# Performance work log

Hardware: AMD Instinct MI355X
Metric: run time of the kernel (lower is better)

The kernel has to match this reference:

```python
import jax, jax.numpy as jnp
import numpy as np

BSZ, NW, T = 16, 1024, 3072   # batch, max words per seq, padded byte length
BED, WED = 128, 512           # byte_embed_dim, word_embed_dim
NH = 2                        # highway layers per block
VOCAB = 256 + 4 + 4
BPE_MASK_IDX = 4


def _conv1d(x, W, b):
    # x: [B, T, Cin], W: [k, Cin, Cout]
    y = jax.lax.conv_general_dilated(x, W, window_strides=(1,), padding='SAME',
                                     dimension_numbers=('NWC', 'WIO', 'NWC'))
    return y + b


def _highway(x, Ws, bs):
    # Ws: [NH, 2D, D], bs: [NH, 2D]; AllenNLP-style highway
    for i in range(NH):
        proj = x @ Ws[i].T + bs[i]
        h, g = jnp.split(proj, 2, axis=-1)
        g = jax.nn.sigmoid(g)
        x = g * jax.nn.relu(h) + (1.0 - g) * x
    return x


def setup_inputs() -> dict:
    rng = np.random.default_rng(0)
    pool_lengths = rng.integers(1, 4, size=(BSZ, NW)).astype(np.int64)  # all >=1 -> npools == NW
    src_lengths = pool_lengths.sum(axis=1)
    byte_tokens = np.zeros((BSZ, T), dtype=np.int64)
    for b in range(BSZ):
        L = int(src_lengths[b])
        byte_tokens[b, :L] = rng.integers(4, 260, size=L)
    pos = np.arange(T)[None, :]
    bpe_mask = (rng.random((BSZ, T)) < 0.3) & (pos < src_lengths[:, None])

    key = jax.random.key(0)
    ks = jax.random.split(key, 12)
    s = 0.02
    tok_emb = jax.random.normal(ks[0], (VOCAB, BED), jnp.float32) * s
    tok_emb = tok_emb.at[0].set(0.0)  # padding_idx = 0
    return {
        'byte_tokens': jnp.asarray(byte_tokens),
        'bpe_mask': jnp.asarray(bpe_mask),
        'pool_lengths': jnp.asarray(pool_lengths),
        'tok_emb': tok_emb,
        'conv0_W': jax.random.normal(ks[1], (3, BED, WED), jnp.float32) * s,
        'conv0_b': jnp.zeros((WED,), jnp.float32),
        'conv1_W': jax.random.normal(ks[2], (3, WED, WED), jnp.float32) * s,
        'conv1_b': jnp.zeros((WED,), jnp.float32),
        'hw0_W': jax.random.normal(ks[3], (NH, 2 * WED, WED), jnp.float32) * s,
        'hw0_b': jnp.zeros((NH, 2 * WED), jnp.float32),
        'hw1_W': jax.random.normal(ks[4], (NH, 2 * WED, WED), jnp.float32) * s,
        'hw1_b': jnp.zeros((NH, 2 * WED), jnp.float32),
        'proj_W': jax.random.normal(ks[5], (WED, WED), jnp.float32) * s,
        'proj_b': jnp.zeros((WED,), jnp.float32),
    }


def reference(byte_tokens, bpe_mask, pool_lengths, tok_emb,
              conv0_W, conv0_b, conv1_W, conv1_b,
              hw0_W, hw0_b, hw1_W, hw1_b, proj_W, proj_b):
    # byte embedding + bpe-marker embedding (index 0 row is zero => no-op where mask is False)
    x = tok_emb[byte_tokens] + tok_emb[jnp.where(bpe_mask, BPE_MASK_IDX, 0)]
    # ConvHighway block 0 (no residual)
    x = _highway(jax.nn.relu(_conv1d(x, conv0_W, conv0_b)), hw0_W, hw0_b)
    # ConvHighway block 1 (residual_conv=True); dropout is identity in eval
    x = _highway(jax.nn.relu(_conv1d(x, conv1_W, conv1_b)) + x, hw1_W, hw1_b)

    # ragged per-word max pool via segment_max (replaces the python double loop)
    cum = jnp.cumsum(pool_lengths, axis=1)                 # [B, NW]
    pos = jnp.arange(T)
    seg = jax.vmap(lambda c: jnp.searchsorted(c, pos, side='right'))(cum)  # [B, T]
    src_len = cum[:, -1]
    valid = pos[None, :] < src_len[:, None]
    gid = jnp.where(valid, jnp.arange(BSZ)[:, None] * NW + jnp.clip(seg, 0, NW - 1), BSZ * NW)
    pooled = jax.ops.segment_max(x.reshape(BSZ * T, WED), gid.reshape(-1),
                                 num_segments=BSZ * NW + 1)
    pooled = pooled[:BSZ * NW].reshape(BSZ, NW, WED)
    pooled = jnp.where(jnp.isfinite(pooled), pooled, 0.0)  # empty pools -> 0 like new_zeros
    return pooled @ proj_W.T + proj_b
```

## Files before the change

### kernel.cpp

```cpp
#include <hip/hip_runtime.h>
#include <hip/hip_bf16.h>
#include <math.h>

typedef __attribute__((ext_vector_type(8))) short short8v;
typedef __attribute__((ext_vector_type(4))) float float4v;

namespace {
constexpr int kBSZ = 16;
constexpr int kNW  = 1024;
constexpr int kT   = 3072;
constexpr int kBED = 128;
constexpr int kWED = 512;
constexpr int kR   = kBSZ * kT;
constexpr int kMP  = kBSZ * kNW;
}

__device__ __forceinline__ unsigned short f2b(float x) {
  unsigned int u = __float_as_uint(x);
  u = u + 0x7FFFu + ((u >> 16) & 1u);
  return (unsigned short)(u >> 16);
}
__device__ __forceinline__ float b2f(unsigned short u) {
  return __uint_as_float(((unsigned int)u) << 16);
}

__device__ __forceinline__ void async16(void* l, const void* g) {
  __builtin_amdgcn_global_load_lds(
      (const __attribute__((address_space(1))) void*)g,
      (__attribute__((address_space(3))) void*)l, 16, 0, 0);
}

__global__ __launch_bounds__(256) void k_embed(
    const int* __restrict__ tok, const int* __restrict__ msk,
    const float* __restrict__ emb, unsigned short* __restrict__ out) {
  int idx = blockIdx.x * 256 + threadIdx.x;
  int row = idx >> 5, c4 = idx & 31;
  const float4* e4 = (const float4*)emb;
  float4 a = e4[tok[row] * 32 + c4];
  float4 b = e4[(msk[row] ? 4 : 0) * 32 + c4];
  ushort4 o;
  o.x = f2b(a.x + b.x); o.y = f2b(a.y + b.y);
  o.z = f2b(a.z + b.z); o.w = f2b(a.w + b.w);
  ((ushort4*)out)[idx] = o;
}

__global__ __launch_bounds__(256) void k_wt_conv(
    const float* __restrict__ W, unsigned short* __restrict__ o, int CIN) {
  int idx = blockIdx.x * 256 + threadIdx.x;
  if (idx >= 3 * kWED * CIN) return;
  int k = idx % CIN, n = (idx / CIN) % kWED, dt = idx / (kWED * CIN);
  o[idx] = f2b(W[(long)(dt * CIN + k) * kWED + n]);
}
__global__ __launch_bounds__(256) void k_f2bk(
    const float* __restrict__ in, unsigned short* __restrict__ o, int n) {
  int idx = blockIdx.x * 256 + threadIdx.x;
  if (idx < n) o[idx] = f2b(in[idx]);
}

__global__ void k_cumsum(const int* __restrict__ pl, int* __restrict__ cum) {
  __shared__ int s[kNW];
  int b = blockIdx.x, i = threadIdx.x;
  s[i] = pl[b * kNW + i];
  __syncthreads();
  for (int off = 1; off < kNW; off <<= 1) {
    int cur = s[i];
    int add = (i >= off) ? s[i - off] : 0;
    __syncthreads();
    s[i] = cur + add;
    __syncthreads();
  }
  cum[b * kNW + i] = s[i];
}

template <int CIN, bool RESID>
__global__ __launch_bounds__(256, 2) void k_convm(
    const unsigned short* __restrict__ X,
    const unsigned short* __restrict__ Wt,
    const float* __restrict__ bias,
    const unsigned short* __restrict__ resid,
    const int* __restrict__ cum,
    unsigned short* __restrict__ out) {
  const int row0 = blockIdx.x * 128, n0 = blockIdx.y * 128;
  const int b = row0 / kT;
  const int t0 = row0 % kT;
  if (t0 >= cum[b * kNW + kNW - 1] + 2) return;

  __shared__ short lds[(130 + 384) * 64];
  short* As = lds;
  short* Bs = lds + 130 * 64;
  const int tid = threadIdx.x, wave = tid >> 6, lane = tid & 63;
  const int q = lane >> 4, rr = lane & 15;
  const int jhi = lane >> 3, jlo = lane & 7;
  const bool lo_ok = (t0 > 0), hi_ok = (t0 + 128 < kT);
  const int wr = (wave >> 1) * 64, wc = (wave & 1) * 64;

  float4v acc[4][4] = {};

  for (int k0 = 0; k0 < CIN; k0 += 64) {
#pragma unroll
    for (int i = 0; i < 4; ++i) {
      int o = wave + 4 * i;
      int m = 1 + o * 8 + jhi;
      int c16 = jlo ^ (m & 7);
      async16((char*)As + (1 + o * 8) * 128,
              X + ((long)(row0 + m - 1) * CIN + k0 + c16 * 8));
    }
    if (tid < 16) {
      int m = (tid < 8) ? 0 : 129;
      int u = tid & 7;
      int c16 = u ^ (m & 7);
      bool ok = (tid < 8) ? lo_ok : hi_ok;
      short8v v = {0, 0, 0, 0, 0, 0, 0, 0};
      if (ok) v = *(const short8v*)(X + ((long)(row0 + m - 1) * CIN + k0 + c16 * 8));
      *(short8v*)((char*)As + m * 128 + u * 16) = v;
    }
#pragma unroll
    for (int i = 0; i < 12; ++i) {
      int o = wave + 4 * i;
      int br = o * 8 + jhi;
      int c16 = jlo ^ (br & 7);
      int dt = br >> 7, n = br & 127;
      async16((char*)Bs + o * 8 * 128,
              Wt + ((long)(dt * kWED + n0 + n) * CIN + k0 + c16 * 8));
    }
    __syncthreads();
#pragma unroll
    for (int dt = 0; dt < 3; ++dt) {
      const int abase = wr + rr + dt;
      const int asw = abase & 7;
      const int bbase = wc + rr;
      const int bsw = rr & 7;
#pragma unroll
      for (int kk = 0; kk < 2; ++kk) {
        short8v a[4], b[4];
#pragma unroll
        for (int mf = 0; mf < 4; ++mf)
          a[mf] = *(const short8v*)((char*)As + (abase + mf * 16) * 128 +
                                    (((kk * 4 + q) ^ asw) * 16));
#pragma unroll
        for (int nf = 0; nf < 4; ++nf)
          b[nf] = *(const short8v*)((char*)Bs + (dt * 128 + bbase + nf * 16) * 128 +
                                    (((kk * 4 + q) ^ bsw) * 16));
#pragma unroll
        for (int mf = 0; mf < 4; ++mf)
#pragma unroll
          for (int nf = 0; nf < 4; ++nf)
            acc[mf][nf] = __builtin_amdgcn_mfma_f32_16x16x32_bf16(
                a[mf], b[nf], acc[mf][nf], 0, 0, 0);
      }
    }
    __syncthreads();
  }
#pragma unroll
  for (int nf = 0; nf < 4; ++nf) {
    int col = n0 + wc + nf * 16 + rr;
    float bv = bias[col];
#pragma unroll
    for (int mf = 0; mf < 4; ++mf)
#pragma unroll
      for (int r = 0; r < 4; ++r) {
        long row = row0 + wr + mf * 16 + q * 4 + r;
        float y = fmaxf(acc[mf][nf][r] + bv, 0.f);
        if (RESID) y += b2f(resid[row * kWED + col]);
        out[row * kWED + col] = f2b(y);
      }
  }
}

__global__ __launch_bounds__(256, 2) void k_hw(
    const unsigned short* __restrict__ X,
    const unsigned short* __restrict__ Wb,
    const float* __restrict__ bias,
    const int* __restrict__ cum,
    unsigned short* __restrict__ out) {
  const int row0 = blockIdx.x * 128, n0 = blockIdx.y * 128;
  const int b = row0 / kT;
  const int t0 = row0 % kT;
  if (t0 >= cum[b * kNW + kNW - 1] + 2) return;

  __shared__ short lds[(128 + 256) * 64];
  short* As = lds;
  short* Bs = lds + 128 * 64;
  const int tid = threadIdx.x, wave = tid >> 6, lane = tid & 63;
  const int q = lane >> 4, rr = lane & 15;
  const int jhi = lane >> 3, jlo = lane & 7;
  const int wr = (wave >> 1) * 64, wc = (wave & 1) * 64;

  float4v acch[4][4] = {}, accg[4][4] = {};

  for (int k0 = 0; k0 < kWED; k0 += 64) {
#pragma unroll
    for (int i = 0; i < 4; ++i) {
      int o = wave + 4 * i;
      int m = o * 8 + jhi;
      int c16 = jlo ^ (m & 7);
      async16((char*)As + o * 8 * 128,
              X + ((long)(row0 + m) * kWED + k0 + c16 * 8));
    }
#pragma unroll
    for (int i = 0; i < 8; ++i) {
      int o = wave + 4 * i;
      int br = o * 8 + jhi;
      int c16 = jlo ^ (br & 7);
      int g = br >> 7, n = br & 127;
      async16((char*)Bs + o * 8 * 128,
              Wb + ((long)(g * 512 + n0 + n) * kWED + k0 + c16 * 8));
    }
    __syncthreads();
    const int abase = wr + rr;
    const int sw = rr & 7;
    const int bbase = wc + rr;
#pragma unroll
    for (int kk = 0; kk < 2; ++kk) {
      short8v a[4], bh[4], bg[4];
#pragma unroll
      for (int mf = 0; mf < 4; ++mf)
        a[mf] = *(const short8v*)((char*)As + (abase + mf * 16) * 128 +
                                  (((kk * 4 + q) ^ sw) * 16));
#pragma unroll
      for (int nf = 0; nf < 4; ++nf) {
        bh[nf] = *(const short8v*)((char*)Bs + (bbase + nf * 16) * 128 +
                                   (((kk * 4 + q) ^ sw) * 16));
        bg[nf] = *(const short8v*)((char*)Bs + (128 + bbase + nf * 16) * 128 +
                                   (((kk * 4 + q) ^ sw) * 16));
      }
#pragma unroll
      for (int mf = 0; mf < 4; ++mf)
#pragma unroll
        for (int nf = 0; nf < 4; ++nf) {
          acch[mf][nf] = __builtin_amdgcn_mfma_f32_16x16x32_bf16(
              a[mf], bh[nf], acch[mf][nf], 0, 0, 0);
          accg[mf][nf] = __builtin_amdgcn_mfma_f32_16x16x32_bf16(
              a[mf], bg[nf], accg[mf][nf], 0, 0, 0);
        }
    }
    __syncthreads();
  }
#pragma unroll
  for (int nf = 0; nf < 4; ++nf) {
    int col = n0 + wc + nf * 16 + rr;
    float bhv = bias[col], bgv = bias[512 + col];
#pragma unroll
    for (int mf = 0; mf < 4; ++mf)
#pragma unroll
      for (int r = 0; r < 4; ++r) {
        long row = row0 + wr + mf * 16 + q * 4 + r;
        float h = fmaxf(acch[mf][nf][r] + bhv, 0.f);
        float g = 1.f / (1.f + __expf(-(accg[mf][nf][r] + bgv)));
        float xv = b2f(X[row * kWED + col]);
        out[row * kWED + col] = f2b(g * h + (1.f - g) * xv);
      }
  }
}

__global__ __launch_bounds__(256, 2) void k_proj(
    const unsigned short* __restrict__ A,
    const unsigned short* __restrict__ Wb,
    const float* __restrict__ bias,
    float* __restrict__ out) {
  __shared__ short lds[(128 + 128) * 64];
  short* As = lds;
  short* Bs = lds + 128 * 64;
  const int tid = threadIdx.x, wave = tid >> 6, lane = tid & 63;
  const int q = lane >> 4, rr = lane & 15;
  const int jhi = lane >> 3, jlo = lane & 7;
  const int row0 = blockIdx.x * 128, n0 = blockIdx.y * 128;
  const int wr = (wave >> 1) * 64, wc = (wave & 1) * 64;

  float4v acc[4][4] = {};

  for (int k0 = 0; k0 < kWED; k0 += 64) {
#pragma unroll
    for (int i = 0; i < 4; ++i) {
      int o = wave + 4 * i;
      int m = o * 8 + jhi;
      int c16 = jlo ^ (m & 7);
      async16((char*)As + o * 8 * 128,
              A + ((long)(row0 + m) * kWED + k0 + c16 * 8));
    }
#pragma unroll
    for (int i = 0; i < 4; ++i) {
      int o = wave + 4 * i;
      int n = o * 8 + jhi;
      int c16 = jlo ^ (n & 7);
      async16((char*)Bs + o * 8 * 128,
              Wb + ((long)(n0 + n) * kWED + k0 + c16 * 8));
    }
    __syncthreads();
    const int abase = wr + rr, bbase = wc + rr;
    const int sw = rr & 7;
#pragma unroll
    for (int kk = 0; kk < 2; ++kk) {
      short8v a[4], b[4];
#pragma unroll
      for (int mf = 0; mf < 4; ++mf)
        a[mf] = *(const short8v*)((char*)As + (abase + mf * 16) * 128 +
                                  (((kk * 4 + q) ^ sw) * 16));
#pragma unroll
      for (int nf = 0; nf < 4; ++nf)
        b[nf] = *(const short8v*)((char*)Bs + (bbase + nf * 16) * 128 +
                                  (((kk * 4 + q) ^ sw) * 16));
#pragma unroll
      for (int mf = 0; mf < 4; ++mf)
#pragma unroll
        for (int nf = 0; nf < 4; ++nf)
          acc[mf][nf] = __builtin_amdgcn_mfma_f32_16x16x32_bf16(
              a[mf], b[nf], acc[mf][nf], 0, 0, 0);
    }
    __syncthreads();
  }
#pragma unroll
  for (int nf = 0; nf < 4; ++nf) {
    int col = n0 + wc + nf * 16 + rr;
    float bv = bias[col];
#pragma unroll
    for (int mf = 0; mf < 4; ++mf)
#pragma unroll
      for (int r = 0; r < 4; ++r) {
        long row = row0 + wr + mf * 16 + q * 4 + r;
        out[row * kWED + col] = acc[mf][nf][r] + bv;
      }
  }
}

__global__ __launch_bounds__(128) void k_pool(
    const unsigned short* __restrict__ x, const int* __restrict__ cum,
    unsigned short* __restrict__ pooled) {
  int bw = blockIdx.x;
  int b = bw >> 10, w = bw & 1023;
  int s = (w == 0) ? 0 : cum[bw - 1];
  int e = cum[bw];
  int c = threadIdx.x;
  float m0 = -INFINITY, m1 = -INFINITY, m2 = -INFINITY, m3 = -INFINITY;
  for (int t = s; t < e; ++t) {
    ushort4 v = ((const ushort4*)(x + (long)(b * kT + t) * kWED))[c];
    m0 = fmaxf(m0, b2f(v.x)); m1 = fmaxf(m1, b2f(v.y));
    m2 = fmaxf(m2, b2f(v.z)); m3 = fmaxf(m3, b2f(v.w));
  }
  if (e <= s) { m0 = m1 = m2 = m3 = 0.f; }
  ushort4 o;
  o.x = f2b(m0); o.y = f2b(m1); o.z = f2b(m2); o.w = f2b(m3);
  ((ushort4*)(pooled + (long)bw * kWED))[c] = o;
}

extern "C" void kernel_launch(void* const* d_in, const int* in_sizes, int n_in,
                              void* d_out, int out_size, void* d_ws, size_t ws_size,
                              hipStream_t stream) {
  (void)in_sizes; (void)n_in; (void)out_size; (void)ws_size;

  const int*   tok = (const int*)d_in[0];
  const int*   msk = (const int*)d_in[1];
  const int*   pl  = (const int*)d_in[2];
  const float* emb = (const float*)d_in[3];
  const float* c0W = (const float*)d_in[4];
  const float* c0b = (const float*)d_in[5];
  const float* c1W = (const float*)d_in[6];
  const float* c1b = (const float*)d_in[7];
  const float* h0W = (const float*)d_in[8];
  const float* h0b = (const float*)d_in[9];
  const float* h1W = (const float*)d_in[10];
  const float* h1b = (const float*)d_in[11];
  const float* pW  = (const float*)d_in[12];
  const float* pb  = (const float*)d_in[13];

  unsigned short* xb0 = (unsigned short*)d_ws;
  unsigned short* xb1 = xb0 + (size_t)kR * kWED;
  unsigned short* cw0 = xb1 + (size_t)kR * kWED;
  unsigned short* cw1 = cw0 + 3 * kWED * kBED;
  unsigned short* hw0 = cw1 + 3 * kWED * kWED;
  unsigned short* hw1 = hw0 + 2 * 1024 * kWED;
  unsigned short* pwb = hw1 + 2 * 1024 * kWED;
  int* cum = (int*)(pwb + kWED * kWED);

  k_cumsum<<<kBSZ, kNW, 0, stream>>>(pl, cum);

  k_wt_conv<<<(3 * kWED * kBED + 255) / 256, 256, 0, stream>>>(c0W, cw0, kBED);
  k_wt_conv<<<(3 * kWED * kWED + 255) / 256, 256, 0, stream>>>(c1W, cw1, kWED);
  k_f2bk<<<(2 * 1024 * kWED + 255) / 256, 256, 0, stream>>>(h0W, hw0, 2 * 1024 * kWED);
  k_f2bk<<<(2 * 1024 * kWED + 255) / 256, 256, 0, stream>>>(h1W, hw1, 2 * 1024 * kWED);
  k_f2bk<<<(kWED * kWED + 255) / 256, 256, 0, stream>>>(pW, pwb, kWED * kWED);

  k_embed<<<kR * 32 / 256, 256, 0, stream>>>(tok, msk, emb, xb0);

  dim3 g1(kR / 128, kWED / 128);

  k_convm<kBED, false><<<g1, 256, 0, stream>>>(xb0, cw0, c0b, nullptr, cum, xb1);
  k_hw<<<g1, 256, 0, stream>>>(xb1, hw0, h0b, cum, xb0);
  k_hw<<<g1, 256, 0, stream>>>(xb0, hw0 + 1024 * kWED, h0b + 1024, cum, xb1);
  k_convm<kWED, true><<<g1, 256, 0, stream>>>(xb1, cw1, c1b, xb1, cum, xb0);
  k_hw<<<g1, 256, 0, stream>>>(xb0, hw1, h1b, cum, xb1);
  k_hw<<<g1, 256, 0, stream>>>(xb1, hw1 + 1024 * kWED, h1b + 1024, cum, xb0);

  k_pool<<<kMP, 128, 0, stream>>>(xb0, cum, xb1);

  dim3 g2(kMP / 128, kWED / 128);
  k_proj<<<g2, 256, 0, stream>>>(xb1, pwb, pb, (float*)d_out);
}
```

Measured before the change: 395.0 us.

## Rewrite highway GEMM as 8-wave double-buffered pipelined kernel with 256-row tiles

Replaces the 4-wave highway GEMM kernel with an 8-wave version that handles 256 rows per block. LDS is double-buffered (128 KB) and the next K-tile is prefetched asynchronously while MFMAs run, using explicit vmcnt/lgkmcnt waits, raw barriers and setprio. The aim is to hide global-load latency and raise MFMA utilisation. The cost is that 128 KB of LDS per block limits occupancy, despite the launch bound of 2, and the hand-written wait counts are fragile.

```diff
diff --git a/kernel.cpp b/kernel.cpp
--- a/kernel.cpp
+++ b/kernel.cpp
@@ -4,6 +4,9 @@
 
 typedef __attribute__((ext_vector_type(8))) short short8v;
 typedef __attribute__((ext_vector_type(4))) float float4v;
+
+#define VMCNT(n) asm volatile("s_waitcnt vmcnt(" #n ")" ::: "memory")
+#define LGK0     asm volatile("s_waitcnt lgkmcnt(0)" ::: "memory")
 
 namespace {
 constexpr int kBSZ = 16;
@@ -167,84 +170,142 @@
   }
 }
 
-__global__ __launch_bounds__(256, 2) void k_hw(
+__global__ __launch_bounds__(512, 2) void k_hw8(
     const unsigned short* __restrict__ X,
     const unsigned short* __restrict__ Wb,
     const float* __restrict__ bias,
     const int* __restrict__ cum,
     unsigned short* __restrict__ out) {
-  const int row0 = blockIdx.x * 128, n0 = blockIdx.y * 128;
-  const int b = row0 / kT;
-  const int t0 = row0 % kT;
-  if (t0 >= cum[b * kNW + kNW - 1] + 2) return;
-
-  __shared__ short lds[(128 + 256) * 64];
-  short* As = lds;
-  short* Bs = lds + 128 * 64;
-  const int tid = threadIdx.x, wave = tid >> 6, lane = tid & 63;
-  const int q = lane >> 4, rr = lane & 15;
-  const int jhi = lane >> 3, jlo = lane & 7;
-  const int wr = (wave >> 1) * 64, wc = (wave & 1) * 64;
-
-  float4v acch[4][4] = {}, accg[4][4] = {};
-
-  for (int k0 = 0; k0 < kWED; k0 += 64) {
-#pragma unroll
-    for (int i = 0; i < 4; ++i) {
-      int o = wave + 4 * i;
-      int m = o * 8 + jhi;
-      int c16 = jlo ^ (m & 7);
-      async16((char*)As + o * 8 * 128,
-              X + ((long)(row0 + m) * kWED + k0 + c16 * 8));
-    }
-#pragma unroll
-    for (int i = 0; i < 8; ++i) {
-      int o = wave + 4 * i;
-      int br = o * 8 + jhi;
-      int c16 = jlo ^ (br & 7);
-      int g = br >> 7, n = br & 127;
-      async16((char*)Bs + o * 8 * 128,
-              Wb + ((long)(g * 512 + n0 + n) * kWED + k0 + c16 * 8));
-    }
-    __syncthreads();
-    const int abase = wr + rr;
-    const int sw = rr & 7;
-    const int bbase = wc + rr;
-#pragma unroll
-    for (int kk = 0; kk < 2; ++kk) {
-      short8v a[4], bh[4], bg[4];
-#pragma unroll
-      for (int mf = 0; mf < 4; ++mf)
-        a[mf] = *(const short8v*)((char*)As + (abase + mf * 16) * 128 +
-                                  (((kk * 4 + q) ^ sw) * 16));
-#pragma unroll
-      for (int nf = 0; nf < 4; ++nf) {
-        bh[nf] = *(const short8v*)((char*)Bs + (bbase + nf * 16) * 128 +
-                                   (((kk * 4 + q) ^ sw) * 16));
-        bg[nf] = *(const short8v*)((char*)Bs + (128 + bbase + nf * 16) * 128 +
-                                   (((kk * 4 + q) ^ sw) * 16));
-      }
-#pragma unroll
-      for (int mf = 0; mf < 4; ++mf)
-#pragma unroll
-        for (int nf = 0; nf < 4; ++nf) {
-          acch[mf][nf] = __builtin_amdgcn_mfma_f32_16x16x32_bf16(
-              a[mf], bh[nf], acch[mf][nf], 0, 0, 0);
-          accg[mf][nf] = __builtin_amdgcn_mfma_f32_16x16x32_bf16(
-              a[mf], bg[nf], accg[mf][nf], 0, 0, 0);
-        }
-    }
-    __syncthreads();
-  }
-#pragma unroll
-  for (int nf = 0; nf < 4; ++nf) {
+  const int row0 = blockIdx.x * 256, n0 = blockIdx.y * 128;
+  const int bb = row0 / kT, t0 = row0 % kT;
+  if (t0 >= cum[bb * kNW + kNW - 1] + 2) return;
+
+  __shared__ alignas(128) char ldsb[131072];
+
+  const int tid = threadIdx.x;
+  const int wv = tid >> 6, lane = tid & 63;
+  const int ql = lane >> 4, rr = lane & 15;
+  const int wr = (wv >> 2) * 128;
+  const int wc = (wv & 3) * 32;
+  const int sdr = lane >> 2, sl = lane & 3;
+
+  float4v acch[8][2] = {}, accg[8][2] = {};
+  short8v a[8], bh[2], bg[2];
+
+  auto stA = [&](int bf, int kt, int kk) {
+#pragma unroll
+    for (int lh = 0; lh < 2; ++lh) {
+      int dr = lh * 128 + wv * 16 + sdr;
+      int ch = sl ^ ((dr >> 1) & 3);
+      async16(ldsb + bf * 65536 + kk * 32768 + lh * 8192 + wv * 1024,
+              X + (long)(row0 + dr) * kWED + kt * 64 + kk * 32 + ch * 8);
+    }
+  };
+  auto stB = [&](int bf, int kt, int kk) {
+#pragma unroll
+    for (int lh = 0; lh < 2; ++lh) {
+      int dr = lh * 128 + wv * 16 + sdr;
+      int ch = sl ^ ((dr >> 1) & 3);
+      int wrow = n0 + dr + (lh ? 384 : 0);
+      async16(ldsb + bf * 65536 + kk * 32768 + 16384 + lh * 8192 + wv * 1024,
+              Wb + (long)wrow * kWED + kt * 64 + kk * 32 + ch * 8);
+    }
+  };
+  auto ldA = [&](int bf, int kk, int row) {
+    return *(const short8v*)(ldsb + bf * 65536 + kk * 32768 + row * 64 +
+                             ((ql ^ ((row >> 1) & 3)) * 16));
+  };
+  auto ldB = [&](int bf, int kk, int row) {
+    return *(const short8v*)(ldsb + bf * 65536 + kk * 32768 + 16384 + row * 64 +
+                             ((ql ^ ((row >> 1) & 3)) * 16));
+  };
+
+  stA(0, 0, 0); stB(0, 0, 0); stA(0, 0, 1); stB(0, 0, 1);
+  VMCNT(4);
+  __builtin_amdgcn_s_barrier();
+
+  for (int kt = 0; kt < 8; ++kt) {
+    const int bf = kt & 1, nb = bf ^ 1;
+    const bool pf = kt < 7;
+
+#pragma unroll
+    for (int mf = 0; mf < 8; ++mf) a[mf] = ldA(bf, 0, wr + rr + mf * 16);
+#pragma unroll
+    for (int nf = 0; nf < 2; ++nf) bh[nf] = ldB(bf, 0, wc + rr + nf * 16);
+    if (pf) stA(nb, kt + 1, 0);
+    __builtin_amdgcn_s_barrier();
+    LGK0; __builtin_amdgcn_sched_barrier(0);
+    __builtin_amdgcn_s_setprio(1);
+#pragma unroll
+    for (int mf = 0; mf < 8; ++mf)
+#pragma unroll
+      for (int nf = 0; nf < 2; ++nf)
+        acch[mf][nf] = __builtin_amdgcn_mfma_f32_16x16x32_bf16(
+            a[mf], bh[nf], acch[mf][nf], 0, 0, 0);
+    __builtin_amdgcn_s_setprio(0);
+    VMCNT(6);
+    __builtin_amdgcn_s_barrier();
+
+#pragma unroll
+    for (int nf = 0; nf < 2; ++nf) bg[nf] = ldB(bf, 0, 128 + wc + rr + nf * 16);
+    if (pf) stB(nb, kt + 1, 0);
+    __builtin_amdgcn_s_barrier();
+    LGK0; __builtin_amdgcn_sched_barrier(0);
+    __builtin_amdgcn_s_setprio(1);
+#pragma unroll
+    for (int mf = 0; mf < 8; ++mf)
+#pragma unroll
+      for (int nf = 0; nf < 2; ++nf)
+        accg[mf][nf] = __builtin_amdgcn_mfma_f32_16x16x32_bf16(
+            a[mf], bg[nf], accg[mf][nf], 0, 0, 0);
+    __builtin_amdgcn_s_setprio(0);
+    VMCNT(4);
+    __builtin_amdgcn_s_barrier();
+
+#pragma unroll
+    for (int mf = 0; mf < 8; ++mf) a[mf] = ldA(bf, 1, wr + rr + mf * 16);
+#pragma unroll
+    for (int nf = 0; nf < 2; ++nf) bh[nf] = ldB(bf, 1, wc + rr + nf * 16);
+    if (pf) stA(nb, kt + 1, 1);
+    __builtin_amdgcn_s_barrier();
+    LGK0; __builtin_amdgcn_sched_barrier(0);
+    __builtin_amdgcn_s_setprio(1);
+#pragma unroll
+    for (int mf = 0; mf < 8; ++mf)
+#pragma unroll
+      for (int nf = 0; nf < 2; ++nf)
+        acch[mf][nf] = __builtin_amdgcn_mfma_f32_16x16x32_bf16(
+            a[mf], bh[nf], acch[mf][nf], 0, 0, 0);
+    __builtin_amdgcn_s_setprio(0);
+    VMCNT(6);
+    __builtin_amdgcn_s_barrier();
+
+#pragma unroll
+    for (int nf = 0; nf < 2; ++nf) bg[nf] = ldB(bf, 1, 128 + wc + rr + nf * 16);
+    if (pf) stB(nb, kt + 1, 1);
+    __builtin_amdgcn_s_barrier();
+    LGK0; __builtin_amdgcn_sched_barrier(0);
+    __builtin_amdgcn_s_setprio(1);
+#pragma unroll
+    for (int mf = 0; mf < 8; ++mf)
+#pragma unroll
+      for (int nf = 0; nf < 2; ++nf)
+        accg[mf][nf] = __builtin_amdgcn_mfma_f32_16x16x32_bf16(
+            a[mf], bg[nf], accg[mf][nf], 0, 0, 0);
+    __builtin_amdgcn_s_setprio(0);
+    VMCNT(4);
+    __builtin_amdgcn_s_barrier();
+  }
+
+#pragma unroll
+  for (int nf = 0; nf < 2; ++nf) {
     int col = n0 + wc + nf * 16 + rr;
     float bhv = bias[col], bgv = bias[512 + col];
 #pragma unroll
-    for (int mf = 0; mf < 4; ++mf)
+    for (int mf = 0; mf < 8; ++mf)
 #pragma unroll
       for (int r = 0; r < 4; ++r) {
-        long row = row0 + wr + mf * 16 + q * 4 + r;
+        long row = row0 + wr + mf * 16 + ql * 4 + r;
         float h = fmaxf(acch[mf][nf][r] + bhv, 0.f);
         float g = 1.f / (1.f + __expf(-(accg[mf][nf][r] + bgv)));
         float xv = b2f(X[row * kWED + col]);
@@ -383,13 +444,14 @@
   k_embed<<<kR * 32 / 256, 256, 0, stream>>>(tok, msk, emb, xb0);
 
   dim3 g1(kR / 128, kWED / 128);
+  dim3 gh(kR / 256, kWED / 128);
 
   k_convm<kBED, false><<<g1, 256, 0, stream>>>(xb0, cw0, c0b, nullptr, cum, xb1);
-  k_hw<<<g1, 256, 0, stream>>>(xb1, hw0, h0b, cum, xb0);
-  k_hw<<<g1, 256, 0, stream>>>(xb0, hw0 + 1024 * kWED, h0b + 1024, cum, xb1);
+  k_hw8<<<gh, 512, 0, stream>>>(xb1, hw0, h0b, cum, xb0);
+  k_hw8<<<gh, 512, 0, stream>>>(xb0, hw0 + 1024 * kWED, h0b + 1024, cum, xb1);
   k_convm<kWED, true><<<g1, 256, 0, stream>>>(xb1, cw1, c1b, xb1, cum, xb0);
-  k_hw<<<g1, 256, 0, stream>>>(xb0, hw1, h1b, cum, xb1);
-  k_hw<<<g1, 256, 0, stream>>>(xb1, hw1 + 1024 * kWED, h1b + 1024, cum, xb0);
+  k_hw8<<<gh, 512, 0, stream>>>(xb0, hw1, h1b, cum, xb1);
+  k_hw8<<<gh, 512, 0, stream>>>(xb1, hw1 + 1024 * kWED, h1b + 1024, cum, xb0);
 
   k_pool<<<kMP, 128, 0, stream>>>(xb0, cum, xb1);
 
```

After: 407.1 us. 3.1% more time.

## Double-buffer LDS with BK=32 tiles in conv, highway and projection GEMMs

Applied to the files above, without the earlier changes.

Converts the three MFMA GEMM kernels from a single-buffered BK=64 loop to a double-buffered BK=32 loop. The next K-slice is prefetched asynchronously into the other LDS buffer while MFMAs run on the current one, so each iteration needs one barrier instead of two. The XOR swizzle is dropped for a plain 64-byte row layout. Conv halo rows are loaded into registers early and written to LDS after compute. The unswizzled layout may cause LDS bank conflicts, and the smaller K step doubles the iteration count.

```diff
diff --git a/kernel.cpp b/kernel.cpp
--- a/kernel.cpp
+++ b/kernel.cpp
@@ -81,76 +81,82 @@
     const int* __restrict__ cum,
     unsigned short* __restrict__ out) {
   const int row0 = blockIdx.x * 128, n0 = blockIdx.y * 128;
-  const int b = row0 / kT;
-  const int t0 = row0 % kT;
+  const int b = row0 / kT, t0 = row0 % kT;
   if (t0 >= cum[b * kNW + kNW - 1] + 2) return;
 
-  __shared__ short lds[(130 + 384) * 64];
-  short* As = lds;
-  short* Bs = lds + 130 * 64;
+  constexpr int NT = CIN / 32;
+  __shared__ short lds[2][(130 + 384) * 32];
   const int tid = threadIdx.x, wave = tid >> 6, lane = tid & 63;
   const int q = lane >> 4, rr = lane & 15;
-  const int jhi = lane >> 3, jlo = lane & 7;
+  const int dr = lane >> 2, sl = lane & 3;
   const bool lo_ok = (t0 > 0), hi_ok = (t0 + 128 < kT);
   const int wr = (wave >> 1) * 64, wc = (wave & 1) * 64;
 
   float4v acc[4][4] = {};
-
-  for (int k0 = 0; k0 < CIN; k0 += 64) {
-#pragma unroll
-    for (int i = 0; i < 4; ++i) {
-      int o = wave + 4 * i;
-      int m = 1 + o * 8 + jhi;
-      int c16 = jlo ^ (m & 7);
-      async16((char*)As + (1 + o * 8) * 128,
-              X + ((long)(row0 + m - 1) * CIN + k0 + c16 * 8));
-    }
-    if (tid < 16) {
-      int m = (tid < 8) ? 0 : 129;
-      int u = tid & 7;
-      int c16 = u ^ (m & 7);
-      bool ok = (tid < 8) ? lo_ok : hi_ok;
+  short8v hv = {0, 0, 0, 0, 0, 0, 0, 0};
+  const int hch = tid & 3;
+  const long hrow = (tid < 4) ? (long)(row0 - 1) : (long)(row0 + 128);
+  const bool hok = (tid < 4) ? lo_ok : hi_ok;
+
+  auto stage = [&](int nb, int k0) {
+    short* As = lds[nb];
+    short* Bs = lds[nb] + 130 * 32;
+#pragma unroll
+    for (int i = 0; i < 2; ++i) {
+      int r0 = (wave + 4 * i) * 16;
+      async16((char*)As + (1 + r0) * 64,
+              X + (long)(row0 + r0 + dr) * CIN + k0 + sl * 8);
+    }
+#pragma unroll
+    for (int i = 0; i < 6; ++i) {
+      int r0 = (wave + 4 * i) * 16;
+      int br = r0 + dr;
+      int dt = br >> 7, n = br & 127;
+      async16((char*)Bs + r0 * 64,
+              Wt + ((long)(dt * kWED + n0 + n)) * CIN + k0 + sl * 8);
+    }
+    if (tid < 8) {
       short8v v = {0, 0, 0, 0, 0, 0, 0, 0};
-      if (ok) v = *(const short8v*)(X + ((long)(row0 + m - 1) * CIN + k0 + c16 * 8));
-      *(short8v*)((char*)As + m * 128 + u * 16) = v;
-    }
-#pragma unroll
-    for (int i = 0; i < 12; ++i) {
-      int o = wave + 4 * i;
-      int br = o * 8 + jhi;
-      int c16 = jlo ^ (br & 7);
-      int dt = br >> 7, n = br & 127;
-      async16((char*)Bs + o * 8 * 128,
-              Wt + ((long)(dt * kWED + n0 + n) * CIN + k0 + c16 * 8));
-    }
+      if (hok) v = *(const short8v*)(X + hrow * CIN + k0 + hch * 8);
+      hv = v;
+    }
+  };
+  auto halo_write = [&](int nb) {
+    if (tid < 8) {
+      int r = (tid < 4) ? 0 : 129;
+      *(short8v*)((char*)lds[nb] + r * 64 + hch * 16) = hv;
+    }
+  };
+
+  stage(0, 0);
+  halo_write(0);
+  __syncthreads();
+
+  for (int t = 0; t < NT; ++t) {
+    const int cur = t & 1, nb = cur ^ 1;
+    if (t + 1 < NT) stage(nb, (t + 1) * 32);
+    const char* As = (const char*)lds[cur];
+    const char* Bs = (const char*)(lds[cur] + 130 * 32);
+#pragma unroll
+    for (int dt = 0; dt < 3; ++dt) {
+      short8v a[4], bb[4];
+#pragma unroll
+      for (int mf = 0; mf < 4; ++mf)
+        a[mf] = *(const short8v*)(As + (wr + rr + dt + mf * 16) * 64 + q * 16);
+#pragma unroll
+      for (int nf = 0; nf < 4; ++nf)
+        bb[nf] = *(const short8v*)(Bs + (dt * 128 + wc + rr + nf * 16) * 64 + q * 16);
+#pragma unroll
+      for (int mf = 0; mf < 4; ++mf)
+#pragma unroll
+        for (int nf = 0; nf < 4; ++nf)
+          acc[mf][nf] = __builtin_amdgcn_mfma_f32_16x16x32_bf16(
+              a[mf], bb[nf], acc[mf][nf], 0, 0, 0);
+    }
+    if (t + 1 < NT) halo_write(nb);
     __syncthreads();
-#pragma unroll
-    for (int dt = 0; dt < 3; ++dt) {
-      const int abase = wr + rr + dt;
-      const int asw = abase & 7;
-      const int bbase = wc + rr;
-      const int bsw = rr & 7;
-#pragma unroll
-      for (int kk = 0; kk < 2; ++kk) {
-        short8v a[4], b[4];
-#pragma unroll
-        for (int mf = 0; mf < 4; ++mf)
-          a[mf] = *(const short8v*)((char*)As + (abase + mf * 16) * 128 +
-                                    (((kk * 4 + q) ^ asw) * 16));
-#pragma unroll
-        for (int nf = 0; nf < 4; ++nf)
-          b[nf] = *(const short8v*)((char*)Bs + (dt * 128 + bbase + nf * 16) * 128 +
-                                    (((kk * 4 + q) ^ bsw) * 16));
-#pragma unroll
-        for (int mf = 0; mf < 4; ++mf)
-#pragma unroll
-          for (int nf = 0; nf < 4; ++nf)
-            acc[mf][nf] = __builtin_amdgcn_mfma_f32_16x16x32_bf16(
-                a[mf], b[nf], acc[mf][nf], 0, 0, 0);
-      }
-    }
-    __syncthreads();
-  }
+  }
+
 #pragma unroll
   for (int nf = 0; nf < 4; ++nf) {
     int col = n0 + wc + nf * 16 + rr;
@@ -174,68 +180,65 @@
     const int* __restrict__ cum,
     unsigned short* __restrict__ out) {
   const int row0 = blockIdx.x * 128, n0 = blockIdx.y * 128;
-  const int b = row0 / kT;
-  const int t0 = row0 % kT;
+  const int b = row0 / kT, t0 = row0 % kT;
   if (t0 >= cum[b * kNW + kNW - 1] + 2) return;
 
-  __shared__ short lds[(128 + 256) * 64];
-  short* As = lds;
-  short* Bs = lds + 128 * 64;
+  __shared__ short lds[2][(128 + 256) * 32];
   const int tid = threadIdx.x, wave = tid >> 6, lane = tid & 63;
   const int q = lane >> 4, rr = lane & 15;
-  const int jhi = lane >> 3, jlo = lane & 7;
+  const int dr = lane >> 2, sl = lane & 3;
   const int wr = (wave >> 1) * 64, wc = (wave & 1) * 64;
 
   float4v acch[4][4] = {}, accg[4][4] = {};
 
-  for (int k0 = 0; k0 < kWED; k0 += 64) {
+  auto stage = [&](int nb, int k0) {
+    short* As = lds[nb];
+    short* Bs = lds[nb] + 128 * 32;
+#pragma unroll
+    for (int i = 0; i < 2; ++i) {
+      int r0 = (wave + 4 * i) * 16;
+      async16((char*)As + r0 * 64,
+              X + (long)(row0 + r0 + dr) * kWED + k0 + sl * 8);
+    }
 #pragma unroll
     for (int i = 0; i < 4; ++i) {
-      int o = wave + 4 * i;
-      int m = o * 8 + jhi;
-      int c16 = jlo ^ (m & 7);
-      async16((char*)As + o * 8 * 128,
-              X + ((long)(row0 + m) * kWED + k0 + c16 * 8));
-    }
-#pragma unroll
-    for (int i = 0; i < 8; ++i) {
-      int o = wave + 4 * i;
-      int br = o * 8 + jhi;
-      int c16 = jlo ^ (br & 7);
+      int r0 = (wave + 4 * i) * 16;
+      int br = r0 + dr;
       int g = br >> 7, n = br & 127;
-      async16((char*)Bs + o * 8 * 128,
-              Wb + ((long)(g * 512 + n0 + n) * kWED + k0 + c16 * 8));
-    }
+      async16((char*)Bs + r0 * 64,
+              Wb + ((long)(g * 512 + n0 + n)) * kWED + k0 + sl * 8);
+    }
+  };
+
+  stage(0, 0);
+  __syncthreads();
+
+  for (int t = 0; t < 16; ++t) {
+    const int cur = t & 1, nb = cur ^ 1;
+    if (t + 1 < 16) stage(nb, (t + 1) * 32);
+    const char* As = (const char*)lds[cur];
+    const char* Bs = (const char*)(lds[cur] + 128 * 32);
+    short8v a[4], bh[4], bg[4];
+#pragma unroll
+    for (int mf = 0; mf < 4; ++mf)
+      a[mf] = *(const short8v*)(As + (wr + rr + mf * 16) * 64 + q * 16);
+#pragma unroll
+    for (int nf = 0; nf < 4; ++nf) {
+      bh[nf] = *(const short8v*)(Bs + (wc + rr + nf * 16) * 64 + q * 16);
+      bg[nf] = *(const short8v*)(Bs + (128 + wc + rr + nf * 16) * 64 + q * 16);
+    }
+#pragma unroll
+    for (int mf = 0; mf < 4; ++mf)
+#pragma unroll
+      for (int nf = 0; nf < 4; ++nf) {
+        acch[mf][nf] = __builtin_amdgcn_mfma_f32_16x16x32_bf16(
+            a[mf], bh[nf], acch[mf][nf], 0, 0, 0);
+        accg[mf][nf] = __builtin_amdgcn_mfma_f32_16x16x32_bf16(
+            a[mf], bg[nf], accg[mf][nf], 0, 0, 0);
+      }
     __syncthreads();
-    const int abase = wr + rr;
-    const int sw = rr & 7;
-    const int bbase = wc + rr;
-#pragma unroll
-    for (int kk = 0; kk < 2; ++kk) {
-      short8v a[4], bh[4], bg[4];
-#pragma unroll
-      for (int mf = 0; mf < 4; ++mf)
-        a[mf] = *(const short8v*)((char*)As + (abase + mf * 16) * 128 +
-                                  (((kk * 4 + q) ^ sw) * 16));
-#pragma unroll
-      for (int nf = 0; nf < 4; ++nf) {
-        bh[nf] = *(const short8v*)((char*)Bs + (bbase + nf * 16) * 128 +
-                                   (((kk * 4 + q) ^ sw) * 16));
-        bg[nf] = *(const short8v*)((char*)Bs + (128 + bbase + nf * 16) * 128 +
-                                   (((kk * 4 + q) ^ sw) * 16));
-      }
-#pragma unroll
-      for (int mf = 0; mf < 4; ++mf)
-#pragma unroll
-        for (int nf = 0; nf < 4; ++nf) {
-          acch[mf][nf] = __builtin_amdgcn_mfma_f32_16x16x32_bf16(
-              a[mf], bh[nf], acch[mf][nf], 0, 0, 0);
-          accg[mf][nf] = __builtin_amdgcn_mfma_f32_16x16x32_bf16(
-              a[mf], bg[nf], accg[mf][nf], 0, 0, 0);
-        }
-    }
-    __syncthreads();
-  }
+  }
+
 #pragma unroll
   for (int nf = 0; nf < 4; ++nf) {
     int col = n0 + wc + nf * 16 + rr;
@@ -258,57 +261,56 @@
     const unsigned short* __restrict__ Wb,
     const float* __restrict__ bias,
     float* __restrict__ out) {
-  __shared__ short lds[(128 + 128) * 64];
-  short* As = lds;
-  short* Bs = lds + 128 * 64;
+  __shared__ short lds[2][(128 + 128) * 32];
   const int tid = threadIdx.x, wave = tid >> 6, lane = tid & 63;
   const int q = lane >> 4, rr = lane & 15;
-  const int jhi = lane >> 3, jlo = lane & 7;
+  const int dr = lane >> 2, sl = lane & 3;
   const int row0 = blockIdx.x * 128, n0 = blockIdx.y * 128;
   const int wr = (wave >> 1) * 64, wc = (wave & 1) * 64;
 
   float4v acc[4][4] = {};
 
-  for (int k0 = 0; k0 < kWED; k0 += 64) {
-#pragma unroll
-    for (int i = 0; i < 4; ++i) {
-      int o = wave + 4 * i;
-      int m = o * 8 + jhi;
-      int c16 = jlo ^ (m & 7);
-      async16((char*)As + o * 8 * 128,
-              A + ((long)(row0 + m) * kWED + k0 + c16 * 8));
-    }
-#pragma unroll
-    for (int i = 0; i < 4; ++i) {
-      int o = wave + 4 * i;
-      int n = o * 8 + jhi;
-      int c16 = jlo ^ (n & 7);
-      async16((char*)Bs + o * 8 * 128,
-              Wb + ((long)(n0 + n) * kWED + k0 + c16 * 8));
-    }
+  auto stage = [&](int nb, int k0) {
+    short* As = lds[nb];
+    short* Bs = lds[nb] + 128 * 32;
+#pragma unroll
+    for (int i = 0; i < 2; ++i) {
+      int r0 = (wave + 4 * i) * 16;
+      async16((char*)As + r0 * 64,
+              A + (long)(row0 + r0 + dr) * kWED + k0 + sl * 8);
+    }
+#pragma unroll
+    for (int i = 0; i < 2; ++i) {
+      int r0 = (wave + 4 * i) * 16;
+      async16((char*)Bs + r0 * 64,
+              Wb + (long)(n0 + r0 + dr) * kWED + k0 + sl * 8);
+    }
+  };
+
+  stage(0, 0);
+  __syncthreads();
+
+  for (int t = 0; t < 16; ++t) {
+    const int cur = t & 1, nb = cur ^ 1;
+    if (t + 1 < 16) stage(nb, (t + 1) * 32);
+    const char* As = (const char*)lds[cur];
+    const char* Bs = (const char*)(lds[cur] + 128 * 32);
+    short8v a[4], bb[4];
+#pragma unroll
+    for (int mf = 0; mf < 4; ++mf)
+      a[mf] = *(const short8v*)(As + (wr + rr + mf * 16) * 64 + q * 16);
+#pragma unroll
+    for (int nf = 0; nf < 4; ++nf)
+      bb[nf] = *(const short8v*)(Bs + (wc + rr + nf * 16) * 64 + q * 16);
+#pragma unroll
+    for (int mf = 0; mf < 4; ++mf)
+#pragma unroll
+      for (int nf = 0; nf < 4; ++nf)
+        acc[mf][nf] = __builtin_amdgcn_mfma_f32_16x16x32_bf16(
+            a[mf], bb[nf], acc[mf][nf], 0, 0, 0);
     __syncthreads();
-    const int abase = wr + rr, bbase = wc + rr;
-    const int sw = rr & 7;
-#pragma unroll
-    for (int kk = 0; kk < 2; ++kk) {
-      short8v a[4], b[4];
-#pragma unroll
-      for (int mf = 0; mf < 4; ++mf)
-        a[mf] = *(const short8v*)((char*)As + (abase + mf * 16) * 128 +
-                                  (((kk * 4 + q) ^ sw) * 16));
-#pragma unroll
-      for (int nf = 0; nf < 4; ++nf)
-        b[nf] = *(const short8v*)((char*)Bs + (bbase + nf * 16) * 128 +
-                                  (((kk * 4 + q) ^ sw) * 16));
-#pragma unroll
-      for (int mf = 0; mf < 4; ++mf)
-#pragma unroll
-        for (int nf = 0; nf < 4; ++nf)
-          acc[mf][nf] = __builtin_amdgcn_mfma_f32_16x16x32_bf16(
-              a[mf], b[nf], acc[mf][nf], 0, 0, 0);
-    }
-    __syncthreads();
-  }
+  }
+
 #pragma unroll
   for (int nf = 0; nf < 4; ++nf) {
     int col = n0 + wc + nf * 16 + rr;
```

Result: slower. 429.3 us (+8.7%).
